# Performance work log

Hardware: AMD Instinct MI355X
Metric: run time of the kernel (lower is better)

The kernel has to match this reference:

```python
import jax, jax.numpy as jnp
import numpy as np

EMB, HEADS = 1024, 16
HEAD_DIM = EMB // HEADS


def _linear(x, W, b):
    # torch nn.Linear convention: x @ W.T + b, W: [out, in]
    return jnp.einsum('bse,oe->bso', x, W) + b


def setup_inputs() -> dict:
    key = jax.random.key(0)
    ks = jax.random.split(key, 11)
    B, S = 2, 2048
    sc = 1.0 / np.sqrt(EMB)
    inp = {
        'x': jax.random.normal(ks[0], (B, S, EMB), dtype=jnp.float32),
        'y': jax.random.normal(ks[1], (B, S, EMB), dtype=jnp.float32),
        'mask': jnp.ones((B, S, S), dtype=jnp.int32),
        'Wq': jax.random.normal(ks[2], (EMB, EMB), dtype=jnp.float32) * sc,
        'bq': jax.random.normal(ks[3], (EMB,), dtype=jnp.float32) * sc,
        'Wk': jax.random.normal(ks[4], (EMB, EMB), dtype=jnp.float32) * sc,
        'bk': jax.random.normal(ks[5], (EMB,), dtype=jnp.float32) * sc,
        'Wv': jax.random.normal(ks[6], (EMB, EMB), dtype=jnp.float32) * sc,
        'bv': jax.random.normal(ks[7], (EMB,), dtype=jnp.float32) * sc,
        'Wo': jax.random.normal(ks[8], (EMB, EMB), dtype=jnp.float32) * sc,
        'bo': jax.random.normal(ks[9], (EMB,), dtype=jnp.float32) * sc,
    }
    return inp


def reference(x, y, mask, Wq, bq, Wk, bk, Wv, bv, Wo, bo):
    B, S, _ = x.shape
    q = _linear(x, Wq, bq).reshape(B, S, HEADS, HEAD_DIM).transpose(0, 2, 1, 3)
    k = _linear(y, Wk, bk).reshape(B, -1, HEADS, HEAD_DIM).transpose(0, 2, 1, 3)
    v = _linear(y, Wv, bv).reshape(B, -1, HEADS, HEAD_DIM).transpose(0, 2, 1, 3)
    # scores: [B, H, Sq, Sk]
    score = jnp.einsum('bhqd,bhkd->bhqk', q, k) / jnp.sqrt(jnp.float32(HEAD_DIM))
    # NOTE: original torch code calls score.masked_fill(...) without assignment,
    # so the mask has no effect on the computation (faithfully ignored here).
    weights = jax.nn.softmax(score, axis=-1)
    attn = jnp.einsum('bhqk,bhkd->bhqd', weights, v)
    attn = attn.transpose(0, 2, 1, 3).reshape(B, S, EMB)
    # dropout is identity in eval mode
    return _linear(attn, Wo, bo)
```

## Files before the change

kernel.cpp:

```cpp
#include <hip/hip_runtime.h>
#include <cstdint>
#include <cstddef>

#define BB 2
#define SS 2048
#define EE 1024
#define HH 16
#define DD 64

typedef __attribute__((ext_vector_type(8))) short short8;
typedef __attribute__((ext_vector_type(4))) short shortx4;
typedef __attribute__((ext_vector_type(8))) unsigned short ushort8;
typedef __attribute__((ext_vector_type(4))) unsigned short ush4;
typedef __attribute__((ext_vector_type(4))) float floatx4;

#define MFMA32(a, b, c) __builtin_amdgcn_mfma_f32_16x16x32_bf16((a), (b), (c), 0, 0, 0)
#define MFMA16(a, b, c) __builtin_amdgcn_mfma_f32_16x16x16bf16_1k((a), (b), (c), 0, 0, 0)

#define QSCALE 0.18033688011112042f

#define G2L16(g, l)                                                        \
    __builtin_amdgcn_global_load_lds(                                      \
        (const __attribute__((address_space(1))) void*)(g),                \
        (__attribute__((address_space(3))) void*)(l), 16, 0, 0)

__device__ __forceinline__ unsigned short f2bf(float f) {
    unsigned int u = __float_as_uint(f);
    u += 0x7fffu + ((u >> 16) & 1u);
    return (unsigned short)(u >> 16);
}

__device__ __forceinline__ unsigned int pkbf(float a, float b) {
    return __builtin_amdgcn_perm(__float_as_uint(b) + 0x8000u,
                                 __float_as_uint(a) + 0x8000u, 0x07060302u);
}

__global__ __launch_bounds__(256) void k_cvt(
    const float* __restrict__ x, unsigned short* __restrict__ xb,
    const float* __restrict__ y, unsigned short* __restrict__ yb,
    const float* __restrict__ w0, unsigned short* __restrict__ d0,
    const float* __restrict__ w1, unsigned short* __restrict__ d1,
    const float* __restrict__ w2, unsigned short* __restrict__ d2,
    const float* __restrict__ w3, unsigned short* __restrict__ d3)
{
    const int g = blockIdx.y;
    if (g >= 2 && blockIdx.x >= 256) return;
    const float* s = (g == 0) ? x : (g == 1) ? y : (g == 2) ? w0
                   : (g == 3) ? w1 : (g == 4) ? w2 : w3;
    unsigned short* d = (g == 0) ? xb : (g == 1) ? yb : (g == 2) ? d0
                      : (g == 3) ? d1 : (g == 4) ? d2 : d3;
    const size_t i = ((size_t)blockIdx.x * 256 + threadIdx.x) * 16;
    floatx4 f0 = *(const floatx4*)(s + i);
    floatx4 f1 = *(const floatx4*)(s + i + 4);
    floatx4 f2 = *(const floatx4*)(s + i + 8);
    floatx4 f3 = *(const floatx4*)(s + i + 12);
    ushort8 o0, o1;
#pragma unroll
    for (int j = 0; j < 4; ++j) { o0[j] = f2bf(f0[j]); o0[j + 4] = f2bf(f1[j]); }
#pragma unroll
    for (int j = 0; j < 4; ++j) { o1[j] = f2bf(f2[j]); o1[j + 4] = f2bf(f3[j]); }
    *(ushort8*)(d + i) = o0;
    *(ushort8*)(d + i + 8) = o1;
}

template <int MT, int OMODE>
__device__ __forceinline__ void gemm_body(
    const unsigned short* __restrict__ A, const unsigned short* __restrict__ W,
    const float* __restrict__ bias, void* __restrict__ Cv, float oscale,
    int m0, int n0, unsigned short* As0, unsigned short* As1,
    unsigned short* Bs0, unsigned short* Bs1)
{
    constexpr int K = 1024, N = 1024, LDT = 32;
    constexpr int MFR = MT / 32;
    const int t = threadIdx.x;
    const int lane = t & 63, w = t >> 6;
    const int q = lane >> 4, c = lane & 15;
    const int wm = w & 1, wn = w >> 1;
    const int lr = lane >> 2, lc = (lane & 3) * 8;

    const unsigned short* gA0 = A + (size_t)(m0 + w * (MT / 4) + lr) * K + lc;
    const unsigned short* gA1 = gA0 + 16 * K;
    unsigned short* lA0_0 = As0 + (w * (MT / 4)) * LDT;
    unsigned short* lA0_1 = lA0_0 + 16 * LDT;
    unsigned short* lA1_0 = As1 + (w * (MT / 4)) * LDT;
    unsigned short* lA1_1 = lA1_0 + 16 * LDT;
    const unsigned short* gB0 = W + (size_t)(n0 + w * 32 + lr) * K + lc;
    const unsigned short* gB1 = gB0 + 16 * K;
    unsigned short* lB0_0 = Bs0 + (w * 32) * LDT;
    unsigned short* lB0_1 = lB0_0 + 16 * LDT;
    unsigned short* lB1_0 = Bs1 + (w * 32) * LDT;
    unsigned short* lB1_1 = lB1_0 + 16 * LDT;

    floatx4 acc[MFR][4] = {};

    for (int kt = 0; kt < K; kt += 64) {
        __syncthreads();
        G2L16(gA0 + kt, lA0_0);
        if constexpr (MT == 128) G2L16(gA1 + kt, lA0_1);
        G2L16(gA0 + kt + 32, lA1_0);
        if constexpr (MT == 128) G2L16(gA1 + kt + 32, lA1_1);
        G2L16(gB0 + kt, lB0_0);
        G2L16(gB1 + kt, lB0_1);
        G2L16(gB0 + kt + 32, lB1_0);
        G2L16(gB1 + kt + 32, lB1_1);
        __syncthreads();

        const unsigned short* Ah[2] = {As0, As1};
        const unsigned short* Bh[2] = {Bs0, Bs1};
#pragma unroll
        for (int hf = 0; hf < 2; ++hf) {
            short8 af[MFR], bfr[4];
#pragma unroll
            for (int mi = 0; mi < MFR; ++mi)
                af[mi] = *(const short8*)
                    &Ah[hf][(wm * (MFR * 16) + mi * 16 + c) * LDT + q * 8];
#pragma unroll
            for (int ni = 0; ni < 4; ++ni)
                bfr[ni] = *(const short8*)
                    &Bh[hf][(wn * 64 + ni * 16 + c) * LDT + q * 8];
#pragma unroll
            for (int mi = 0; mi < MFR; ++mi)
#pragma unroll
                for (int ni = 0; ni < 4; ++ni)
                    acc[mi][ni] = MFMA32(af[mi], bfr[ni], acc[mi][ni]);
        }
    }

#pragma unroll
    for (int ni = 0; ni < 4; ++ni) {
        const int col = n0 + wn * 64 + ni * 16 + c;
        const float bv = bias[col];
#pragma unroll
        for (int mi = 0; mi < MFR; ++mi)
#pragma unroll
            for (int r = 0; r < 4; ++r) {
                const int row = m0 + wm * (MFR * 16) + mi * 16 + q * 4 + r;
                const float v = (acc[mi][ni][r] + bv) * oscale;
                if constexpr (OMODE == 0) {
                    ((unsigned short*)Cv)[(size_t)row * N + col] = f2bf(v);
                } else if constexpr (OMODE == 1) {
                    const int b = row >> 11, s = row & 2047;
                    ((unsigned short*)Cv)[((size_t)(b * 1024 + col)) * SS + s] = f2bf(v);
                } else {
                    ((float*)Cv)[(size_t)row * N + col] = v;
                }
            }
    }
}

__global__ __launch_bounds__(256) void k_gemm_qkv(
    const unsigned short* __restrict__ x, const unsigned short* __restrict__ y,
    const unsigned short* __restrict__ Wq, const float* __restrict__ bq,
    const unsigned short* __restrict__ Wk, const float* __restrict__ bk,
    const unsigned short* __restrict__ Wv, const float* __restrict__ bv,
    unsigned short* __restrict__ Q, unsigned short* __restrict__ Ko,
    unsigned short* __restrict__ Vt)
{
    __shared__ __align__(16) unsigned short As0[128 * 32], As1[128 * 32];
    __shared__ __align__(16) unsigned short Bs0[128 * 32], Bs1[128 * 32];
    const int m0 = blockIdx.y * 128;
    const int nt = blockIdx.x;
    const int g = nt >> 3;
    const int n0 = (nt & 7) * 128;
    if (g == 0) {
        gemm_body<128, 0>(x, Wq, bq, Q, QSCALE, m0, n0, As0, As1, Bs0, Bs1);
    } else if (g == 1) {
        gemm_body<128, 0>(y, Wk, bk, Ko, 1.0f, m0, n0, As0, As1, Bs0, Bs1);
    } else {
        gemm_body<128, 1>(y, Wv, bv, Vt, 1.0f, m0, n0, As0, As1, Bs0, Bs1);
    }
}

__global__ __launch_bounds__(256) void k_gemm_out(
    const unsigned short* __restrict__ A, const unsigned short* __restrict__ W,
    const float* __restrict__ bias, float* __restrict__ C)
{
    __shared__ __align__(16) unsigned short As0[64 * 32], As1[64 * 32];
    __shared__ __align__(16) unsigned short Bs0[128 * 32], Bs1[128 * 32];
    gemm_body<64, 2>(A, W, bias, C, 1.0f, blockIdx.y * 64, blockIdx.x * 128,
                     As0, As1, Bs0, Bs1);
}

__global__ __launch_bounds__(512, 4) void k_attn(
    const unsigned short* __restrict__ Q, const unsigned short* __restrict__ K,
    const unsigned short* __restrict__ Vt, unsigned short* __restrict__ O)
{
    constexpr int LDK = 72;
    __shared__ __align__(16) char smem[34816];
    unsigned short* Ksb = (unsigned short*)smem;
    unsigned short* Vsb = (unsigned short*)(smem + 2 * 64 * LDK * 2);
    float* Ob = (float*)smem;

    const int bh = blockIdx.x, qt = blockIdx.y;
    const int b = bh >> 4, h = bh & 15;
    const int t = threadIdx.x, w = t >> 6;
    const int ws = w >> 2;
    const int wq = w & 3;
    const int lane = t & 63, q = lane >> 4, c = lane & 15;

    unsigned short* Ks = Ksb + ws * (64 * LDK);
    unsigned short* Vs = Vsb + ws * (64 * 64);

    short8 qb[2][2];
#pragma unroll
    for (int g = 0; g < 2; ++g) {
        const size_t qoff =
            (size_t)(b * SS + qt * 128 + wq * 32 + g * 16 + c) * EE + h * DD + q * 8;
        qb[g][0] = *(const short8*)(Q + qoff);
        qb[g][1] = *(const short8*)(Q + qoff + 32);
    }

    floatx4 o[2][4] = {};
    floatx4 lacc[2] = {};
    const shortx4 ones = {(short)0x3F80, (short)0x3F80, (short)0x3F80, (short)0x3F80};

    const int ts = t & 255;
    const int sr = ts >> 2, sp = (ts & 3) * 16;
    const int vkey = (sr & 15) << 2;
    const unsigned short* Kg =
        K + (size_t)(b * SS + ws * 1024 + sr) * EE + h * DD + sp;
    const unsigned short* Vg =
        Vt + ((size_t)bh * DD + sr) * SS + ws * 1024 + sp;

    for (int kt = 0; kt < 1024; kt += 64) {
        __syncthreads();
        {
            const ushort8* gk = (const ushort8*)(Kg + (size_t)kt * EE);
            ushort8 k0 = gk[0], k1 = gk[1];
            *(ushort8*)&Ks[sr * LDK + sp] = k0;
            *(ushort8*)&Ks[sr * LDK + sp + 8] = k1;
            const ushort8* gv = (const ushort8*)(Vg + kt);
            ushort8 v0 = gv[0], v1 = gv[1];
            *(ush4*)&Vs[sr * 64 + ((sp +  0) ^ vkey)] =
                __builtin_shufflevector(v0, v0, 0, 1, 2, 3);
            *(ush4*)&Vs[sr * 64 + ((sp +  4) ^ vkey)] =
                __builtin_shufflevector(v0, v0, 4, 5, 6, 7);
            *(ush4*)&Vs[sr * 64 + ((sp +  8) ^ vkey)] =
                __builtin_shufflevector(v1, v1, 0, 1, 2, 3);
            *(ush4*)&Vs[sr * 64 + ((sp + 12) ^ vkey)] =
                __builtin_shufflevector(v1, v1, 4, 5, 6, 7);
        }
        __syncthreads();

        shortx4 pa[2][4];
#pragma unroll
        for (int tt = 0; tt < 4; ++tt) {
            const short8 ka0 = *(const short8*)&Ks[(tt * 16 + c) * LDK + q * 8];
            const short8 ka1 = *(const short8*)&Ks[(tt * 16 + c) * LDK + 32 + q * 8];
#pragma unroll
            for (int g = 0; g < 2; ++g) {
                floatx4 s = {0.f, 0.f, 0.f, 0.f};
                s = MFMA32(ka0, qb[g][0], s);
                s = MFMA32(ka1, qb[g][1], s);
                union { unsigned int u[2]; shortx4 v; } pk;
                pk.u[0] = pkbf(exp2f(s[0]), exp2f(s[1]));
                pk.u[1] = pkbf(exp2f(s[2]), exp2f(s[3]));
                pa[g][tt] = pk.v;
            }
        }

#pragma unroll
        for (int nd = 0; nd < 4; ++nd)
#pragma unroll
            for (int tt = 0; tt < 4; ++tt) {
                const shortx4 vb = *(const shortx4*)
                    &Vs[(nd * 16 + c) * 64 + (((tt * 4 + q) ^ c) << 2)];
                o[0][nd] = MFMA16(pa[0][tt], vb, o[0][nd]);
                o[1][nd] = MFMA16(pa[1][tt], vb, o[1][nd]);
            }
#pragma unroll
        for (int tt = 0; tt < 4; ++tt) {
            lacc[0] = MFMA16(pa[0][tt], ones, lacc[0]);
            lacc[1] = MFMA16(pa[1][tt], ones, lacc[1]);
        }
    }

    __syncthreads();
    if (ws == 1) {
#pragma unroll
        for (int g = 0; g < 2; ++g) {
#pragma unroll
            for (int nd = 0; nd < 4; ++nd)
#pragma unroll
                for (int r = 0; r < 4; ++r)
                    Ob[(wq * 32 + g * 16 + q * 4 + r) * 66 + nd * 16 + c] =
                        o[g][nd][r];
            if (c == 0) {
#pragma unroll
                for (int r = 0; r < 4; ++r)
                    Ob[(wq * 32 + g * 16 + q * 4 + r) * 66 + 64] = lacc[g][r];
            }
        }
    }
    __syncthreads();
    if (ws == 0) {
#pragma unroll
        for (int g = 0; g < 2; ++g) {
            float linv[4];
#pragma unroll
            for (int r = 0; r < 4; ++r) {
                const int rr = wq * 32 + g * 16 + q * 4 + r;
#pragma unroll
                for (int nd = 0; nd < 4; ++nd)
                    o[g][nd][r] += Ob[rr * 66 + nd * 16 + c];
                linv[r] = __builtin_amdgcn_rcpf(lacc[g][r] + Ob[rr * 66 + 64]);
            }
            const int orow = b * SS + qt * 128 + wq * 32 + g * 16;
#pragma unroll
            for (int nd = 0; nd < 4; ++nd)
#pragma unroll
                for (int r = 0; r < 4; ++r)
                    O[(size_t)(orow + q * 4 + r) * EE + h * DD + nd * 16 + c] =
                        f2bf(o[g][nd][r] * linv[r]);
        }
    }
}

extern "C" void kernel_launch(void* const* d_in, const int* in_sizes, int n_in,
                              void* d_out, int out_size, void* d_ws, size_t ws_size,
                              hipStream_t stream)
{
    const float* x  = (const float*)d_in[0];
    const float* y  = (const float*)d_in[1];
    const float* Wq = (const float*)d_in[3];
    const float* bq = (const float*)d_in[4];
    const float* Wk = (const float*)d_in[5];
    const float* bk = (const float*)d_in[6];
    const float* Wv = (const float*)d_in[7];
    const float* bv = (const float*)d_in[8];
    const float* Wo = (const float*)d_in[9];
    const float* bo = (const float*)d_in[10];
    float* out = (float*)d_out;

    char* ws = (char*)d_ws;
    const size_t SZ = (size_t)BB * SS * EE * sizeof(unsigned short);
    const size_t WZ = (size_t)EE * EE * sizeof(unsigned short);
    unsigned short* xb  = (unsigned short*)(ws);
    unsigned short* yb  = (unsigned short*)(ws + SZ);
    unsigned short* Wqb = (unsigned short*)(ws + 2 * SZ);
    unsigned short* Wkb = (unsigned short*)(ws + 2 * SZ + WZ);
    unsigned short* Wvb = (unsigned short*)(ws + 2 * SZ + 2 * WZ);
    unsigned short* Wob = (unsigned short*)(ws + 2 * SZ + 3 * WZ);
    unsigned short* Qw  = (unsigned short*)(ws + 2 * SZ + 4 * WZ);
    unsigned short* Kw  = (unsigned short*)(ws + 3 * SZ + 4 * WZ);
    unsigned short* Vtw = (unsigned short*)(ws + 4 * SZ + 4 * WZ);
    unsigned short* Aw  = (unsigned short*)(ws + 5 * SZ + 4 * WZ);
    (void)ws_size; (void)in_sizes; (void)n_in; (void)out_size;

    k_cvt<<<dim3(1024, 6), 256, 0, stream>>>(x, xb, y, yb, Wq, Wqb, Wk, Wkb,
                                             Wv, Wvb, Wo, Wob);
    k_gemm_qkv<<<dim3(24, 32), 256, 0, stream>>>(xb, yb, Wqb, bq, Wkb, bk, Wvb, bv,
                                                 Qw, Kw, Vtw);
    k_attn<<<dim3(32, 16), 512, 0, stream>>>(Qw, Kw, Vtw, Aw);
    k_gemm_out<<<dim3(8, 64), 256, 0, stream>>>(Aw, Wob, bo, out);
}
```

Before: 244.0 us.

## Double-buffer K/V tiles in attention with register prefetch and MFMA priority

Reworks the attention kernel's key loop to use two LDS buffers per key-split half. The next K/V tile is loaded into registers before computing on the current one, then written to the alternate buffer afterwards, which removes one of the two barriers per iteration. The MFMA section is also wrapped in s_setprio so waves doing matrix work get issue priority. The cost is doubled LDS use (about 69KB versus 35KB), which may reduce blocks per CU, more live registers, and a wasted wraparound prefetch on the last iteration.

```diff
diff --git a/kernel.cpp b/kernel.cpp
--- a/kernel.cpp
+++ b/kernel.cpp
@@ -186,9 +186,8 @@
     const unsigned short* __restrict__ Vt, unsigned short* __restrict__ O)
 {
     constexpr int LDK = 72;
-    __shared__ __align__(16) char smem[34816];
-    unsigned short* Ksb = (unsigned short*)smem;
-    unsigned short* Vsb = (unsigned short*)(smem + 2 * 64 * LDK * 2);
+    constexpr int TSZ = 64 * LDK + 64 * 64;
+    __shared__ __align__(16) unsigned short smem[2 * 2 * TSZ];
     float* Ob = (float*)smem;
 
     const int bh = blockIdx.x, qt = blockIdx.y;
@@ -198,8 +197,7 @@
     const int wq = w & 3;
     const int lane = t & 63, q = lane >> 4, c = lane & 15;
 
-    unsigned short* Ks = Ksb + ws * (64 * LDK);
-    unsigned short* Vs = Vsb + ws * (64 * 64);
+    unsigned short* Sb = smem + ws * (2 * TSZ);
 
     short8 qb[2][2];
 #pragma unroll
@@ -222,25 +220,38 @@
     const unsigned short* Vg =
         Vt + ((size_t)bh * DD + sr) * SS + ws * 1024 + sp;
 
-    for (int kt = 0; kt < 1024; kt += 64) {
+    {
+        const ushort8* gk = (const ushort8*)Kg;
+        ushort8 k0 = gk[0], k1 = gk[1];
+        const ushort8* gv = (const ushort8*)Vg;
+        ushort8 v0 = gv[0], v1 = gv[1];
+        unsigned short* Ks = Sb;
+        unsigned short* Vs = Sb + 64 * LDK;
+        *(ushort8*)&Ks[sr * LDK + sp] = k0;
+        *(ushort8*)&Ks[sr * LDK + sp + 8] = k1;
+        *(ush4*)&Vs[sr * 64 + ((sp +  0) ^ vkey)] =
+            __builtin_shufflevector(v0, v0, 0, 1, 2, 3);
+        *(ush4*)&Vs[sr * 64 + ((sp +  4) ^ vkey)] =
+            __builtin_shufflevector(v0, v0, 4, 5, 6, 7);
+        *(ush4*)&Vs[sr * 64 + ((sp +  8) ^ vkey)] =
+            __builtin_shufflevector(v1, v1, 0, 1, 2, 3);
+        *(ush4*)&Vs[sr * 64 + ((sp + 12) ^ vkey)] =
+            __builtin_shufflevector(v1, v1, 4, 5, 6, 7);
+    }
+
+    for (int it = 0; it < 16; ++it) {
+        const unsigned short* Ks = Sb + (it & 1) * TSZ;
+        const unsigned short* Vs = Ks + 64 * LDK;
         __syncthreads();
+
+        const int nit = (it + 1) & 15;
+        ushort8 pk0, pk1, pv0, pv1;
         {
-            const ushort8* gk = (const ushort8*)(Kg + (size_t)kt * EE);
-            ushort8 k0 = gk[0], k1 = gk[1];
-            *(ushort8*)&Ks[sr * LDK + sp] = k0;
-            *(ushort8*)&Ks[sr * LDK + sp + 8] = k1;
-            const ushort8* gv = (const ushort8*)(Vg + kt);
-            ushort8 v0 = gv[0], v1 = gv[1];
-            *(ush4*)&Vs[sr * 64 + ((sp +  0) ^ vkey)] =
-                __builtin_shufflevector(v0, v0, 0, 1, 2, 3);
-            *(ush4*)&Vs[sr * 64 + ((sp +  4) ^ vkey)] =
-                __builtin_shufflevector(v0, v0, 4, 5, 6, 7);
-            *(ush4*)&Vs[sr * 64 + ((sp +  8) ^ vkey)] =
-                __builtin_shufflevector(v1, v1, 0, 1, 2, 3);
-            *(ush4*)&Vs[sr * 64 + ((sp + 12) ^ vkey)] =
-                __builtin_shufflevector(v1, v1, 4, 5, 6, 7);
-        }
-        __syncthreads();
+            const ushort8* gk = (const ushort8*)(Kg + (size_t)nit * 64 * EE);
+            pk0 = gk[0]; pk1 = gk[1];
+            const ushort8* gv = (const ushort8*)(Vg + nit * 64);
+            pv0 = gv[0]; pv1 = gv[1];
+        }
 
         shortx4 pa[2][4];
 #pragma unroll
@@ -259,6 +270,7 @@
             }
         }
 
+        __builtin_amdgcn_s_setprio(1);
 #pragma unroll
         for (int nd = 0; nd < 4; ++nd)
 #pragma unroll
@@ -272,6 +284,22 @@
         for (int tt = 0; tt < 4; ++tt) {
             lacc[0] = MFMA16(pa[0][tt], ones, lacc[0]);
             lacc[1] = MFMA16(pa[1][tt], ones, lacc[1]);
+        }
+        __builtin_amdgcn_s_setprio(0);
+
+        {
+            unsigned short* Kn = Sb + ((it + 1) & 1) * TSZ;
+            unsigned short* Vn = Kn + 64 * LDK;
+            *(ushort8*)&Kn[sr * LDK + sp] = pk0;
+            *(ushort8*)&Kn[sr * LDK + sp + 8] = pk1;
+            *(ush4*)&Vn[sr * 64 + ((sp +  0) ^ vkey)] =
+                __builtin_shufflevector(pv0, pv0, 0, 1, 2, 3);
+            *(ush4*)&Vn[sr * 64 + ((sp +  4) ^ vkey)] =
+                __builtin_shufflevector(pv0, pv0, 4, 5, 6, 7);
+            *(ush4*)&Vn[sr * 64 + ((sp +  8) ^ vkey)] =
+                __builtin_shufflevector(pv1, pv1, 0, 1, 2, 3);
+            *(ush4*)&Vn[sr * 64 + ((sp + 12) ^ vkey)] =
+                __builtin_shufflevector(pv1, pv1, 4, 5, 6, 7);
         }
     }
 
```

Result: no change. 240.4 us (-1.5%).
